# Kernel tuning notes

Hardware: AMD Instinct MI355X
Metric: run time of the kernel (lower is better)

The kernel has to match this reference:

```python
import jax, jax.numpy as jnp
import numpy as np


def setup_inputs() -> dict:
    key = jax.random.key(0)
    ks = jax.random.split(key, 5)
    B, M, R = 32, 32, 128
    d_lang, d_region, d_rank, d_fusion = 1024, 2048, 256, 256
    u = jax.random.normal(ks[0], (B, M, d_lang), dtype=jnp.float32)
    v = jax.random.normal(ks[1], (B, R, d_region), dtype=jnp.float32)
    # Linear weights stored torch-style as (out_features, in_features)
    Wu = jax.random.normal(ks[2], (d_rank, d_lang), dtype=jnp.float32) * (1.0 / np.sqrt(d_lang))
    Wv = jax.random.normal(ks[3], (d_rank, d_region), dtype=jnp.float32) * (1.0 / np.sqrt(d_region))
    Wp = jax.random.normal(ks[4], (d_fusion, d_rank), dtype=jnp.float32) * (1.0 / np.sqrt(d_rank))
    bp = jnp.zeros((d_fusion,), dtype=jnp.float32)
    return {"u": u, "v": v, "Wu": Wu, "Wv": Wv, "Wp": Wp, "bp": bp}


def reference(u, v, Wu, Wv, Wp, bp):
    # u: (B, M, d_lang), v: (B, R, d_region)
    up = jnp.einsum('bmd,rd->bmr', u, Wu)          # (B, M, d_rank)  [rd: out x in]
    vp = jnp.einsum('bnd,rd->bnr', v, Wv)          # (B, R, d_rank)
    # broadcast bilinear multiply: (B, M, R, d_rank)
    prod = up[:, :, None, :] * vp[:, None, :, :]
    o = jnp.einsum('bmnk,fk->bmnf', prod, Wp) + bp  # p-linear -> (B, M, R, d_fusion)
    # dropout is identity in inference mode
    return jax.nn.relu(o)
```

## Files before the change

kernel.cpp:

```cpp
#include <hip/hip_runtime.h>
#include <hip/hip_bf16.h>


typedef __attribute__((ext_vector_type(8))) short short8;
typedef __attribute__((ext_vector_type(4))) float floatx4;
typedef __attribute__((ext_vector_type(4))) unsigned uintx4;

__device__ __forceinline__ short f2bf(float f) {
    union { float f; unsigned u; } cv; cv.f = f;
    unsigned r = cv.u + 0x7fffu + ((cv.u >> 16) & 1u);
    return (short)(r >> 16);
}
__device__ __forceinline__ unsigned pack_rne(float x, float y) {
    __hip_bfloat162 h = __float22bfloat162_rn(make_float2(x, y));
    union { __hip_bfloat162 h; unsigned u; } cv; cv.h = h;
    return cv.u;
}

#define GL2LDS(gptr, lptr) __builtin_amdgcn_global_load_lds(                    \
    (const __attribute__((address_space(1))) void*)(gptr),                      \
    (__attribute__((address_space(3))) void*)(lptr), 16, 0, 0)

#define MFMA16(a, b, c) __builtin_amdgcn_mfma_f32_16x16x32_bf16((a), (b), (c), 0, 0, 0)

__global__ __launch_bounds__(256) void proj_kernel(
    const float* __restrict__ u, const float* __restrict__ Wu,
    float* __restrict__ upf,
    const float* __restrict__ v, const float* __restrict__ Wv,
    short* __restrict__ vpb)
{
    __shared__ __align__(16) short Xs[2][64 * 128];
    __shared__ __align__(16) short Wsh[2][64 * 128];

    const int tid  = threadIdx.x;
    const int lane = tid & 63;
    const int wave = tid >> 6;
    const int quad = lane >> 4;
    const int l15  = lane & 15;

    const int bid = blockIdx.x;
    const float *X, *W;
    int D, rb, cb;
    bool is_u;
    if (bid < 64) {
        is_u = true; X = u; W = Wu; D = 1024;
        const int xcd = bid & 7, j = bid >> 3;
        cb = j & 3; rb = (j >> 2) * 8 + xcd;
    } else {
        is_u = false; X = v; W = Wv; D = 2048;
        const int lb = bid - 64;
        const int xcd = lb & 7, j = lb >> 3;
        cb = j & 3; rb = (j >> 2) * 8 + xcd;
    }
    const int r0 = rb * 64, c0 = cb * 64;
    const int wr = (wave >> 1) * 32;
    const int wc = (wave & 1) * 32;

    const int sr = tid >> 2;
    const int sc = (tid & 3) * 32;
    const float* xg = X + (size_t)(r0 + sr) * D + sc;
    const float* wg = W + (size_t)(c0 + sr) * D + sc;
    const int swz   = (sr & 7) << 4;
    const int rbase = sr * 256 + sc * 2;

    floatx4 acc[2][2] = {};

    float4 x0, x1, x2, x3, x4, x5, x6, x7;
    float4 y0, y1, y2, y3, y4, y5, y6, y7;

#define LDC(koff)                                                               \
    x0 = *(const float4*)(xg + (koff));      x1 = *(const float4*)(xg + (koff) + 4);  \
    x2 = *(const float4*)(xg + (koff) + 8);  x3 = *(const float4*)(xg + (koff) + 12); \
    x4 = *(const float4*)(xg + (koff) + 16); x5 = *(const float4*)(xg + (koff) + 20); \
    x6 = *(const float4*)(xg + (koff) + 24); x7 = *(const float4*)(xg + (koff) + 28); \
    y0 = *(const float4*)(wg + (koff));      y1 = *(const float4*)(wg + (koff) + 4);  \
    y2 = *(const float4*)(wg + (koff) + 8);  y3 = *(const float4*)(wg + (koff) + 12); \
    y4 = *(const float4*)(wg + (koff) + 16); y5 = *(const float4*)(wg + (koff) + 20); \
    y6 = *(const float4*)(wg + (koff) + 24); y7 = *(const float4*)(wg + (koff) + 28);

#define PKC(bufi)                                                               \
    { char* xb = (char*)&Xs[bufi][0]; char* wb = (char*)&Wsh[bufi][0];          \
      uintx4 q;                                                                 \
      q[0] = pack_rne(x0.x, x0.y); q[1] = pack_rne(x0.z, x0.w);                 \
      q[2] = pack_rne(x1.x, x1.y); q[3] = pack_rne(x1.z, x1.w);                 \
      *(uintx4*)(xb + ((rbase +  0) ^ swz)) = q;                                \
      q[0] = pack_rne(x2.x, x2.y); q[1] = pack_rne(x2.z, x2.w);                 \
      q[2] = pack_rne(x3.x, x3.y); q[3] = pack_rne(x3.z, x3.w);                 \
      *(uintx4*)(xb + ((rbase + 16) ^ swz)) = q;                                \
      q[0] = pack_rne(x4.x, x4.y); q[1] = pack_rne(x4.z, x4.w);                 \
      q[2] = pack_rne(x5.x, x5.y); q[3] = pack_rne(x5.z, x5.w);                 \
      *(uintx4*)(xb + ((rbase + 32) ^ swz)) = q;                                \
      q[0] = pack_rne(x6.x, x6.y); q[1] = pack_rne(x6.z, x6.w);                 \
      q[2] = pack_rne(x7.x, x7.y); q[3] = pack_rne(x7.z, x7.w);                 \
      *(uintx4*)(xb + ((rbase + 48) ^ swz)) = q;                                \
      q[0] = pack_rne(y0.x, y0.y); q[1] = pack_rne(y0.z, y0.w);                 \
      q[2] = pack_rne(y1.x, y1.y); q[3] = pack_rne(y1.z, y1.w);                 \
      *(uintx4*)(wb + ((rbase +  0) ^ swz)) = q;                                \
      q[0] = pack_rne(y2.x, y2.y); q[1] = pack_rne(y2.z, y2.w);                 \
      q[2] = pack_rne(y3.x, y3.y); q[3] = pack_rne(y3.z, y3.w);                 \
      *(uintx4*)(wb + ((rbase + 16) ^ swz)) = q;                                \
      q[0] = pack_rne(y4.x, y4.y); q[1] = pack_rne(y4.z, y4.w);                 \
      q[2] = pack_rne(y5.x, y5.y); q[3] = pack_rne(y5.z, y5.w);                 \
      *(uintx4*)(wb + ((rbase + 32) ^ swz)) = q;                                \
      q[0] = pack_rne(y6.x, y6.y); q[1] = pack_rne(y6.z, y6.w);                 \
      q[2] = pack_rne(y7.x, y7.y); q[3] = pack_rne(y7.z, y7.w);                 \
      *(uintx4*)(wb + ((rbase + 48) ^ swz)) = q; }

    LDC(0);
    PKC(0);
    __syncthreads();

    const int aswz = (l15 & 7) << 4;
    int cur = 0;
    for (int kc = 0; kc < D; kc += 128) {
        const bool has = (kc + 128) < D;
        if (has) { LDC(kc + 128); }

        const char* xr  = (const char*)&Xs[cur][0];
        const char* wrb = (const char*)&Wsh[cur][0];
#pragma unroll
        for (int ks = 0; ks < 4; ks++) {
            const int co = ks * 64 + quad * 16;
            short8 a0 = *(const short8*)(xr  + (((wr +      l15) * 256 + co) ^ aswz));
            short8 a1 = *(const short8*)(xr  + (((wr + 16 + l15) * 256 + co) ^ aswz));
            short8 b0 = *(const short8*)(wrb + (((wc +      l15) * 256 + co) ^ aswz));
            short8 b1 = *(const short8*)(wrb + (((wc + 16 + l15) * 256 + co) ^ aswz));
            acc[0][0] = MFMA16(a0, b0, acc[0][0]);
            acc[0][1] = MFMA16(a0, b1, acc[0][1]);
            acc[1][0] = MFMA16(a1, b0, acc[1][0]);
            acc[1][1] = MFMA16(a1, b1, acc[1][1]);
        }
        if (has) { PKC(cur ^ 1); }
        __syncthreads();
        cur ^= 1;
    }
#undef LDC
#undef PKC

    if (is_u) {
#pragma unroll
        for (int tn = 0; tn < 2; tn++)
#pragma unroll
            for (int tf = 0; tf < 2; tf++)
#pragma unroll
                for (int r = 0; r < 4; r++) {
                    const int row = r0 + wr + tn * 16 + quad * 4 + r;
                    const int col = c0 + wc + tf * 16 + l15;
                    upf[(size_t)row * 256 + col] = acc[tn][tf][r];
                }
    } else {
#pragma unroll
        for (int tn = 0; tn < 2; tn++)
#pragma unroll
            for (int tf = 0; tf < 2; tf++)
#pragma unroll
                for (int r = 0; r < 4; r++) {
                    const int row = r0 + wr + tn * 16 + quad * 4 + r;
                    const int col = c0 + wc + tf * 16 + l15;
                    vpb[(size_t)row * 256 + col] = f2bf(acc[tn][tf][r]);
                }
    }
}

__global__ __launch_bounds__(256) void bilinear_kernel(
    const float* __restrict__ up, const short* __restrict__ vp,
    const float* __restrict__ Wp, const float* __restrict__ bp,
    float* __restrict__ out)
{
    __shared__ __align__(16) short vp_s[2][128 * 32];
    __shared__ __align__(16) short Ws[2][128 * 32];
    __shared__ float up_s[256];

    const int tid  = threadIdx.x;
    const int lane = tid & 63;
    const int wave = tid >> 6;
    const int quad = lane >> 4;
    const int l15  = lane & 15;

    const int bid = blockIdx.x;
    const int xcd = bid & 7;
    const int grp = bid >> 3;
    const int s   = grp & 63;
    const int b   = (grp >> 6) * 8 + xcd;
    const int m   = s >> 1;
    const int f_blk = s & 1;
    const int bm  = b * 32 + m;
    const int f0  = f_blk * 128;
    const int wn  = (wave >> 1) * 64;
    const int wf  = (wave & 1) * 64;

    const int sr  = tid >> 2;
    const int skg = (tid & 3) * 8;
    const int sn  = tid >> 1;
    const int skh = (tid & 1) * 16;

    up_s[tid] = up[(size_t)bm * 256 + tid];

    const short* vg = vp + (size_t)(b * 128 + sr) * 256 + skg;
    const float* wq = Wp + (size_t)(f0 + sn) * 256 + skh;

    GL2LDS(vg,            &vp_s[0][sr * 32 + skg]);
    GL2LDS(vg + 64 * 256, &vp_s[0][(64 + sr) * 32 + skg]);
    float4 w0 = *(const float4*)wq;
    float4 w1 = *(const float4*)(wq + 4);
    float4 w2 = *(const float4*)(wq + 8);
    float4 w3 = *(const float4*)(wq + 12);
    __syncthreads();
    {
        const float* us = &up_s[skh];
        float4 u0 = *(const float4*)us,       u1 = *(const float4*)(us + 4),
               u2 = *(const float4*)(us + 8), u3 = *(const float4*)(us + 12);
        uintx4 o0, o1;
        o0[0] = pack_rne(w0.x * u0.x, w0.y * u0.y);
        o0[1] = pack_rne(w0.z * u0.z, w0.w * u0.w);
        o0[2] = pack_rne(w1.x * u1.x, w1.y * u1.y);
        o0[3] = pack_rne(w1.z * u1.z, w1.w * u1.w);
        o1[0] = pack_rne(w2.x * u2.x, w2.y * u2.y);
        o1[1] = pack_rne(w2.z * u2.z, w2.w * u2.w);
        o1[2] = pack_rne(w3.x * u3.x, w3.y * u3.y);
        o1[3] = pack_rne(w3.z * u3.z, w3.w * u3.w);
        *(uintx4*)&Ws[0][sn * 32 + skh]     = o0;
        *(uintx4*)&Ws[0][sn * 32 + skh + 8] = o1;
    }
    __syncthreads();

    floatx4 acc[4][4] = {};

#pragma unroll
    for (int kc = 0; kc < 256; kc += 32) {
        const int cur = (kc >> 5) & 1;
        const int nxt = cur ^ 1;
        const bool has = kc < 224;
        float4 v0, v1, v2, v3;
        if (has) {
            const short* g = vg + kc + 32;
            GL2LDS(g,            &vp_s[nxt][sr * 32 + skg]);
            GL2LDS(g + 64 * 256, &vp_s[nxt][(64 + sr) * 32 + skg]);
            const float* wqn = wq + kc + 32;
            v0 = *(const float4*)wqn;       v1 = *(const float4*)(wqn + 4);
            v2 = *(const float4*)(wqn + 8); v3 = *(const float4*)(wqn + 12);
        }

        short8 a[4], bb[4];
#pragma unroll
        for (int tt = 0; tt < 4; tt++)
            a[tt] = *(const short8*)&vp_s[cur][(wn + tt * 16 + l15) * 32 + quad * 8];
#pragma unroll
        for (int tt = 0; tt < 4; tt++)
            bb[tt] = *(const short8*)&Ws[cur][(wf + tt * 16 + l15) * 32 + quad * 8];
#pragma unroll
        for (int tn = 0; tn < 4; tn++)
#pragma unroll
            for (int tf = 0; tf < 4; tf++)
                acc[tn][tf] = MFMA16(a[tn], bb[tf], acc[tn][tf]);

        if (has) {
            const float* us = &up_s[kc + 32 + skh];
            float4 u0 = *(const float4*)us,       u1 = *(const float4*)(us + 4),
                   u2 = *(const float4*)(us + 8), u3 = *(const float4*)(us + 12);
            uintx4 o0, o1;
            o0[0] = pack_rne(v0.x * u0.x, v0.y * u0.y);
            o0[1] = pack_rne(v0.z * u0.z, v0.w * u0.w);
            o0[2] = pack_rne(v1.x * u1.x, v1.y * u1.y);
            o0[3] = pack_rne(v1.z * u1.z, v1.w * u1.w);
            o1[0] = pack_rne(v2.x * u2.x, v2.y * u2.y);
            o1[1] = pack_rne(v2.z * u2.z, v2.w * u2.w);
            o1[2] = pack_rne(v3.x * u3.x, v3.y * u3.y);
            o1[3] = pack_rne(v3.z * u3.z, v3.w * u3.w);
            *(uintx4*)&Ws[nxt][sn * 32 + skh]     = o0;
            *(uintx4*)&Ws[nxt][sn * 32 + skh + 8] = o1;
        }
        __syncthreads();
    }

    float bpv[4];
#pragma unroll
    for (int tf = 0; tf < 4; tf++) bpv[tf] = bp[f0 + wf + tf * 16 + l15];

    const size_t out_base = (size_t)bm * 128 * 256;
#pragma unroll
    for (int tn = 0; tn < 4; tn++)
#pragma unroll
        for (int r = 0; r < 4; r++) {
            const int n = wn + tn * 16 + quad * 4 + r;
            float* op = out + out_base + (size_t)n * 256 + f0 + wf + l15;
#pragma unroll
            for (int tf = 0; tf < 4; tf++) {
                float val = acc[tn][tf][r] + bpv[tf];
                op[tf * 16] = fmaxf(val, 0.0f);
            }
        }
}

extern "C" void kernel_launch(void* const* d_in, const int* in_sizes, int n_in,
                              void* d_out, int out_size, void* d_ws, size_t ws_size,
                              hipStream_t stream) {
    const float* u  = (const float*)d_in[0];
    const float* v  = (const float*)d_in[1];
    const float* Wu = (const float*)d_in[2];
    const float* Wv = (const float*)d_in[3];
    const float* Wp = (const float*)d_in[4];
    const float* bp = (const float*)d_in[5];
    float* out = (float*)d_out;

    float* up_f  = (float*)d_ws;
    short* vp_bf = (short*)(up_f + 262144);

    proj_kernel<<<dim3(320), dim3(256), 0, stream>>>(
        u, Wu, up_f, v, Wv, vp_bf);
    bilinear_kernel<<<dim3(2048), dim3(256), 0, stream>>>(
        up_f, vp_bf, Wp, bp, out);
}
```

Before: 240.0 us.

## Shrink projection tiles and build scaled Wp fragments in registers for bilinear MFMA

The projection kernel now uses 32x64 output tiles with 64-wide K chunks, and the launch grows from 320 to 640 blocks so more CUs are busy. In the bilinear kernel the LDS staging of the up-scaled Wp tile is removed: each lane loads its own Wp rows directly, multiplies them by up values and packs the result into MFMA B fragments in registers. The vp LDS tile gains an XOR swizzle to avoid bank conflicts. The trade-off is more redundant global Wp loads across waves and higher register pressure in exchange for less LDS traffic and fewer LDS writes.

```diff
diff --git a/kernel.cpp b/kernel.cpp
--- a/kernel.cpp
+++ b/kernel.cpp
@@ -29,8 +29,8 @@
     const float* __restrict__ v, const float* __restrict__ Wv,
     short* __restrict__ vpb)
 {
-    __shared__ __align__(16) short Xs[2][64 * 128];
-    __shared__ __align__(16) short Wsh[2][64 * 128];
+    __shared__ __align__(16) short Xs[2][32 * 64];
+    __shared__ __align__(16) short Wsh[2][64 * 64];
 
     const int tid  = threadIdx.x;
     const int lane = tid & 63;
@@ -39,97 +39,67 @@
     const int l15  = lane & 15;
 
     const int bid = blockIdx.x;
-    const float *X, *W;
-    int D, rb, cb;
-    bool is_u;
-    if (bid < 64) {
-        is_u = true; X = u; W = Wu; D = 1024;
-        const int xcd = bid & 7, j = bid >> 3;
-        cb = j & 3; rb = (j >> 2) * 8 + xcd;
-    } else {
-        is_u = false; X = v; W = Wv; D = 2048;
-        const int lb = bid - 64;
-        const int xcd = lb & 7, j = lb >> 3;
-        cb = j & 3; rb = (j >> 2) * 8 + xcd;
-    }
-    const int r0 = rb * 64, c0 = cb * 64;
-    const int wr = (wave >> 1) * 32;
+    const int xcd = bid & 7, j = bid >> 3;
+    const int cb  = j & 3;
+    const int pidx = xcd + 8 * (j >> 2);
+    const float *X, *W; int D, r0; bool is_u;
+    if (pidx < 32) { is_u = true;  X = u; W = Wu; D = 1024; r0 = pidx * 32; }
+    else           { is_u = false; X = v; W = Wv; D = 2048; r0 = (pidx - 32) * 32; }
+    const int c0 = cb * 64;
+    const int wr = (wave >> 1) * 16;
     const int wc = (wave & 1) * 32;
 
-    const int sr = tid >> 2;
-    const int sc = (tid & 3) * 32;
-    const float* xg = X + (size_t)(r0 + sr) * D + sc;
-    const float* wg = W + (size_t)(c0 + sr) * D + sc;
-    const int swz   = (sr & 7) << 4;
-    const int rbase = sr * 256 + sc * 2;
-
-    floatx4 acc[2][2] = {};
-
-    float4 x0, x1, x2, x3, x4, x5, x6, x7;
-    float4 y0, y1, y2, y3, y4, y5, y6, y7;
-
-#define LDC(koff)                                                               \
-    x0 = *(const float4*)(xg + (koff));      x1 = *(const float4*)(xg + (koff) + 4);  \
-    x2 = *(const float4*)(xg + (koff) + 8);  x3 = *(const float4*)(xg + (koff) + 12); \
-    x4 = *(const float4*)(xg + (koff) + 16); x5 = *(const float4*)(xg + (koff) + 20); \
-    x6 = *(const float4*)(xg + (koff) + 24); x7 = *(const float4*)(xg + (koff) + 28); \
-    y0 = *(const float4*)(wg + (koff));      y1 = *(const float4*)(wg + (koff) + 4);  \
-    y2 = *(const float4*)(wg + (koff) + 8);  y3 = *(const float4*)(wg + (koff) + 12); \
-    y4 = *(const float4*)(wg + (koff) + 16); y5 = *(const float4*)(wg + (koff) + 20); \
-    y6 = *(const float4*)(wg + (koff) + 24); y7 = *(const float4*)(wg + (koff) + 28);
-
-#define PKC(bufi)                                                               \
-    { char* xb = (char*)&Xs[bufi][0]; char* wb = (char*)&Wsh[bufi][0];          \
-      uintx4 q;                                                                 \
+    const int xr_ = tid >> 3, xk = (tid & 7) * 8;
+    const int wr_ = tid >> 2, wk = (tid & 3) * 16;
+    const float* xg = X + (size_t)(r0 + xr_) * D + xk;
+    const float* wg = W + (size_t)(c0 + wr_) * D + wk;
+    const int xswz  = (xr_ & 7) << 4;
+    const int wswz  = (wr_ & 7) << 4;
+    const int xbase = xr_ * 128 + xk * 2;
+    const int wbase = wr_ * 128 + wk * 2;
+
+    floatx4 acc[2] = {};
+    float4 x0, x1, y0, y1, y2, y3;
+
+#define LDC(k)                                                                  \
+    x0 = *(const float4*)(xg + (k));      x1 = *(const float4*)(xg + (k) + 4);  \
+    y0 = *(const float4*)(wg + (k));      y1 = *(const float4*)(wg + (k) + 4);  \
+    y2 = *(const float4*)(wg + (k) + 8);  y3 = *(const float4*)(wg + (k) + 12);
+
+#define PKC(bi)                                                                 \
+    { char* xb = (char*)&Xs[bi][0]; char* wb = (char*)&Wsh[bi][0]; uintx4 q;    \
       q[0] = pack_rne(x0.x, x0.y); q[1] = pack_rne(x0.z, x0.w);                 \
       q[2] = pack_rne(x1.x, x1.y); q[3] = pack_rne(x1.z, x1.w);                 \
-      *(uintx4*)(xb + ((rbase +  0) ^ swz)) = q;                                \
-      q[0] = pack_rne(x2.x, x2.y); q[1] = pack_rne(x2.z, x2.w);                 \
-      q[2] = pack_rne(x3.x, x3.y); q[3] = pack_rne(x3.z, x3.w);                 \
-      *(uintx4*)(xb + ((rbase + 16) ^ swz)) = q;                                \
-      q[0] = pack_rne(x4.x, x4.y); q[1] = pack_rne(x4.z, x4.w);                 \
-      q[2] = pack_rne(x5.x, x5.y); q[3] = pack_rne(x5.z, x5.w);                 \
-      *(uintx4*)(xb + ((rbase + 32) ^ swz)) = q;                                \
-      q[0] = pack_rne(x6.x, x6.y); q[1] = pack_rne(x6.z, x6.w);                 \
-      q[2] = pack_rne(x7.x, x7.y); q[3] = pack_rne(x7.z, x7.w);                 \
-      *(uintx4*)(xb + ((rbase + 48) ^ swz)) = q;                                \
+      *(uintx4*)(xb + (xbase ^ xswz)) = q;                                      \
       q[0] = pack_rne(y0.x, y0.y); q[1] = pack_rne(y0.z, y0.w);                 \
       q[2] = pack_rne(y1.x, y1.y); q[3] = pack_rne(y1.z, y1.w);                 \
-      *(uintx4*)(wb + ((rbase +  0) ^ swz)) = q;                                \
+      *(uintx4*)(wb + (wbase ^ wswz)) = q;                                      \
       q[0] = pack_rne(y2.x, y2.y); q[1] = pack_rne(y2.z, y2.w);                 \
       q[2] = pack_rne(y3.x, y3.y); q[3] = pack_rne(y3.z, y3.w);                 \
-      *(uintx4*)(wb + ((rbase + 16) ^ swz)) = q;                                \
-      q[0] = pack_rne(y4.x, y4.y); q[1] = pack_rne(y4.z, y4.w);                 \
-      q[2] = pack_rne(y5.x, y5.y); q[3] = pack_rne(y5.z, y5.w);                 \
-      *(uintx4*)(wb + ((rbase + 32) ^ swz)) = q;                                \
-      q[0] = pack_rne(y6.x, y6.y); q[1] = pack_rne(y6.z, y6.w);                 \
-      q[2] = pack_rne(y7.x, y7.y); q[3] = pack_rne(y7.z, y7.w);                 \
-      *(uintx4*)(wb + ((rbase + 48) ^ swz)) = q; }
-
-    LDC(0);
-    PKC(0);
+      *(uintx4*)(wb + ((wbase + 16) ^ wswz)) = q; }
+
+    LDC(0); PKC(0);
     __syncthreads();
 
-    const int aswz = (l15 & 7) << 4;
+    const int asw = (l15 & 7) << 4;
     int cur = 0;
-    for (int kc = 0; kc < D; kc += 128) {
-        const bool has = (kc + 128) < D;
-        if (has) { LDC(kc + 128); }
-
-        const char* xr  = (const char*)&Xs[cur][0];
-        const char* wrb = (const char*)&Wsh[cur][0];
-#pragma unroll
-        for (int ks = 0; ks < 4; ks++) {
-            const int co = ks * 64 + quad * 16;
-            short8 a0 = *(const short8*)(xr  + (((wr +      l15) * 256 + co) ^ aswz));
-            short8 a1 = *(const short8*)(xr  + (((wr + 16 + l15) * 256 + co) ^ aswz));
-            short8 b0 = *(const short8*)(wrb + (((wc +      l15) * 256 + co) ^ aswz));
-            short8 b1 = *(const short8*)(wrb + (((wc + 16 + l15) * 256 + co) ^ aswz));
-            acc[0][0] = MFMA16(a0, b0, acc[0][0]);
-            acc[0][1] = MFMA16(a0, b1, acc[0][1]);
-            acc[1][0] = MFMA16(a1, b0, acc[1][0]);
-            acc[1][1] = MFMA16(a1, b1, acc[1][1]);
-        }
+    for (int kc = 0; kc < D; kc += 64) {
+        const bool has = (kc + 64) < D;
+        if (has) { LDC(kc + 64); }
+
+        const char* xb = (const char*)&Xs[cur][0];
+        const char* wb = (const char*)&Wsh[cur][0];
+        short8 a0  = *(const short8*)(xb + (((wr + l15) * 128 +      quad * 16) ^ asw));
+        short8 a1  = *(const short8*)(xb + (((wr + l15) * 128 + 64 + quad * 16) ^ asw));
+        short8 b00 = *(const short8*)(wb + (((wc +      l15) * 128 +      quad * 16) ^ asw));
+        short8 b01 = *(const short8*)(wb + (((wc +      l15) * 128 + 64 + quad * 16) ^ asw));
+        short8 b10 = *(const short8*)(wb + (((wc + 16 + l15) * 128 +      quad * 16) ^ asw));
+        short8 b11 = *(const short8*)(wb + (((wc + 16 + l15) * 128 + 64 + quad * 16) ^ asw));
+        acc[0] = MFMA16(a0, b00, acc[0]);
+        acc[1] = MFMA16(a0, b10, acc[1]);
+        acc[0] = MFMA16(a1, b01, acc[0]);
+        acc[1] = MFMA16(a1, b11, acc[1]);
+
         if (has) { PKC(cur ^ 1); }
         __syncthreads();
         cur ^= 1;
@@ -139,26 +109,22 @@
 
     if (is_u) {
 #pragma unroll
-        for (int tn = 0; tn < 2; tn++)
-#pragma unroll
-            for (int tf = 0; tf < 2; tf++)
-#pragma unroll
-                for (int r = 0; r < 4; r++) {
-                    const int row = r0 + wr + tn * 16 + quad * 4 + r;
-                    const int col = c0 + wc + tf * 16 + l15;
-                    upf[(size_t)row * 256 + col] = acc[tn][tf][r];
-                }
+        for (int tf = 0; tf < 2; tf++)
+#pragma unroll
+            for (int r = 0; r < 4; r++) {
+                const int row = r0 + wr + quad * 4 + r;
+                const int col = c0 + wc + tf * 16 + l15;
+                upf[(size_t)row * 256 + col] = acc[tf][r];
+            }
     } else {
 #pragma unroll
-        for (int tn = 0; tn < 2; tn++)
-#pragma unroll
-            for (int tf = 0; tf < 2; tf++)
-#pragma unroll
-                for (int r = 0; r < 4; r++) {
-                    const int row = r0 + wr + tn * 16 + quad * 4 + r;
-                    const int col = c0 + wc + tf * 16 + l15;
-                    vpb[(size_t)row * 256 + col] = f2bf(acc[tn][tf][r]);
-                }
+        for (int tf = 0; tf < 2; tf++)
+#pragma unroll
+            for (int r = 0; r < 4; r++) {
+                const int row = r0 + wr + quad * 4 + r;
+                const int col = c0 + wc + tf * 16 + l15;
+                vpb[(size_t)row * 256 + col] = f2bf(acc[tf][r]);
+            }
     }
 }
 
@@ -168,8 +134,7 @@
     float* __restrict__ out)
 {
     __shared__ __align__(16) short vp_s[2][128 * 32];
-    __shared__ __align__(16) short Ws[2][128 * 32];
-    __shared__ float up_s[256];
+    __shared__ __align__(16) float up_s[256];
 
     const int tid  = threadIdx.x;
     const int lane = tid & 63;
@@ -189,65 +154,69 @@
     const int wn  = (wave >> 1) * 64;
     const int wf  = (wave & 1) * 64;
 
-    const int sr  = tid >> 2;
-    const int skg = (tid & 3) * 8;
-    const int sn  = tid >> 1;
-    const int skh = (tid & 1) * 16;
+    const int sr = tid >> 2, q = tid & 3;
+    const int qg = q ^ ((sr >> 1) & 3);
+    const short* vg0 = vp + (size_t)(b * 128 +      sr) * 256 + qg * 8;
+    const short* vg1 = vp + (size_t)(b * 128 + 64 + sr) * 256 + qg * 8;
 
     up_s[tid] = up[(size_t)bm * 256 + tid];
 
-    const short* vg = vp + (size_t)(b * 128 + sr) * 256 + skg;
-    const float* wq = Wp + (size_t)(f0 + sn) * 256 + skh;
-
-    GL2LDS(vg,            &vp_s[0][sr * 32 + skg]);
-    GL2LDS(vg + 64 * 256, &vp_s[0][(64 + sr) * 32 + skg]);
-    float4 w0 = *(const float4*)wq;
-    float4 w1 = *(const float4*)(wq + 4);
-    float4 w2 = *(const float4*)(wq + 8);
-    float4 w3 = *(const float4*)(wq + 12);
+    const float* wpg = Wp + (size_t)(f0 + wf + l15) * 256 + quad * 8;
+
+    GL2LDS(vg0, &vp_s[0][sr * 32 + q * 8]);
+    GL2LDS(vg1, &vp_s[0][(64 + sr) * 32 + q * 8]);
+    float4 w[4][2];
+#pragma unroll
+    for (int tt = 0; tt < 4; tt++) {
+        w[tt][0] = *(const float4*)(wpg + tt * 4096);
+        w[tt][1] = *(const float4*)(wpg + tt * 4096 + 4);
+    }
     __syncthreads();
-    {
-        const float* us = &up_s[skh];
-        float4 u0 = *(const float4*)us,       u1 = *(const float4*)(us + 4),
-               u2 = *(const float4*)(us + 8), u3 = *(const float4*)(us + 12);
-        uintx4 o0, o1;
-        o0[0] = pack_rne(w0.x * u0.x, w0.y * u0.y);
-        o0[1] = pack_rne(w0.z * u0.z, w0.w * u0.w);
-        o0[2] = pack_rne(w1.x * u1.x, w1.y * u1.y);
-        o0[3] = pack_rne(w1.z * u1.z, w1.w * u1.w);
-        o1[0] = pack_rne(w2.x * u2.x, w2.y * u2.y);
-        o1[1] = pack_rne(w2.z * u2.z, w2.w * u2.w);
-        o1[2] = pack_rne(w3.x * u3.x, w3.y * u3.y);
-        o1[3] = pack_rne(w3.z * u3.z, w3.w * u3.w);
-        *(uintx4*)&Ws[0][sn * 32 + skh]     = o0;
-        *(uintx4*)&Ws[0][sn * 32 + skh + 8] = o1;
-    }
-    __syncthreads();
 
     floatx4 acc[4][4] = {};
+    const int aslot = (quad ^ ((l15 >> 1) & 3)) * 16;
 
 #pragma unroll
     for (int kc = 0; kc < 256; kc += 32) {
         const int cur = (kc >> 5) & 1;
         const int nxt = cur ^ 1;
         const bool has = kc < 224;
-        float4 v0, v1, v2, v3;
+
         if (has) {
-            const short* g = vg + kc + 32;
-            GL2LDS(g,            &vp_s[nxt][sr * 32 + skg]);
-            GL2LDS(g + 64 * 256, &vp_s[nxt][(64 + sr) * 32 + skg]);
-            const float* wqn = wq + kc + 32;
-            v0 = *(const float4*)wqn;       v1 = *(const float4*)(wqn + 4);
-            v2 = *(const float4*)(wqn + 8); v3 = *(const float4*)(wqn + 12);
-        }
-
-        short8 a[4], bb[4];
-#pragma unroll
-        for (int tt = 0; tt < 4; tt++)
-            a[tt] = *(const short8*)&vp_s[cur][(wn + tt * 16 + l15) * 32 + quad * 8];
-#pragma unroll
-        for (int tt = 0; tt < 4; tt++)
-            bb[tt] = *(const short8*)&Ws[cur][(wf + tt * 16 + l15) * 32 + quad * 8];
+            GL2LDS(vg0 + kc + 32, &vp_s[nxt][sr * 32 + q * 8]);
+            GL2LDS(vg1 + kc + 32, &vp_s[nxt][(64 + sr) * 32 + q * 8]);
+        }
+
+        const float4 ua = *(const float4*)&up_s[kc + quad * 8];
+        const float4 ub = *(const float4*)&up_s[kc + quad * 8 + 4];
+        short8 bb[4];
+#pragma unroll
+        for (int tt = 0; tt < 4; tt++) {
+            uintx4 o;
+            o[0] = pack_rne(w[tt][0].x * ua.x, w[tt][0].y * ua.y);
+            o[1] = pack_rne(w[tt][0].z * ua.z, w[tt][0].w * ua.w);
+            o[2] = pack_rne(w[tt][1].x * ub.x, w[tt][1].y * ub.y);
+            o[3] = pack_rne(w[tt][1].z * ub.z, w[tt][1].w * ub.w);
+            union { uintx4 u; short8 s; } cv; cv.u = o;
+            bb[tt] = cv.s;
+        }
+
+        float4 wnx[4][2];
+        if (has) {
+#pragma unroll
+            for (int tt = 0; tt < 4; tt++) {
+                wnx[tt][0] = *(const float4*)(wpg + tt * 4096 + kc + 32);
+                wnx[tt][1] = *(const float4*)(wpg + tt * 4096 + kc + 36);
+            }
+        }
+
+        short8 a[4];
+#pragma unroll
+        for (int tt = 0; tt < 4; tt++) {
+            const int row = wn + tt * 16 + l15;
+            a[tt] = *(const short8*)((const char*)&vp_s[cur][0] + row * 64 + aslot);
+        }
+
 #pragma unroll
         for (int tn = 0; tn < 4; tn++)
 #pragma unroll
@@ -255,20 +224,8 @@
                 acc[tn][tf] = MFMA16(a[tn], bb[tf], acc[tn][tf]);
 
         if (has) {
-            const float* us = &up_s[kc + 32 + skh];
-            float4 u0 = *(const float4*)us,       u1 = *(const float4*)(us + 4),
-                   u2 = *(const float4*)(us + 8), u3 = *(const float4*)(us + 12);
-            uintx4 o0, o1;
-            o0[0] = pack_rne(v0.x * u0.x, v0.y * u0.y);
-            o0[1] = pack_rne(v0.z * u0.z, v0.w * u0.w);
-            o0[2] = pack_rne(v1.x * u1.x, v1.y * u1.y);
-            o0[3] = pack_rne(v1.z * u1.z, v1.w * u1.w);
-            o1[0] = pack_rne(v2.x * u2.x, v2.y * u2.y);
-            o1[1] = pack_rne(v2.z * u2.z, v2.w * u2.w);
-            o1[2] = pack_rne(v3.x * u3.x, v3.y * u3.y);
-            o1[3] = pack_rne(v3.z * u3.z, v3.w * u3.w);
-            *(uintx4*)&Ws[nxt][sn * 32 + skh]     = o0;
-            *(uintx4*)&Ws[nxt][sn * 32 + skh + 8] = o1;
+#pragma unroll
+            for (int tt = 0; tt < 4; tt++) { w[tt][0] = wnx[tt][0]; w[tt][1] = wnx[tt][1]; }
         }
         __syncthreads();
     }
@@ -306,7 +263,7 @@
     float* up_f  = (float*)d_ws;
     short* vp_bf = (short*)(up_f + 262144);
 
-    proj_kernel<<<dim3(320), dim3(256), 0, stream>>>(
+    proj_kernel<<<dim3(640), dim3(256), 0, stream>>>(
         u, Wu, up_f, v, Wv, vp_bf);
     bilinear_kernel<<<dim3(2048), dim3(256), 0, stream>>>(
         up_f, vp_bf, Wp, bp, out);
```

After: 250.7 us. 1.04x slower.
